# Kernel optimization log

Measured on AMD Instinct MI355X. Metric: run time of the kernel, lower is better.

## Reference

```python
import jax, jax.numpy as jnp
import numpy as np

D = 256          # embedding_dim
N_SUPPORT = 320  # n_way * n_shot = 20 * 16
N_QUERY = 2048
N_WAY = 20


def setup_inputs() -> dict:
    key = jax.random.key(0)
    ks = jax.random.split(key, 6)
    scale = 1.0 / np.sqrt(2 * D)
    return {
        "support_embeddings": jax.random.normal(ks[0], (N_SUPPORT, D), dtype=jnp.float32),
        "query_embeddings": jax.random.normal(ks[1], (N_QUERY, D), dtype=jnp.float32),
        "support_labels": jax.random.randint(ks[2], (N_SUPPORT,), 0, N_WAY, dtype=jnp.int64)
            if jax.config.jax_enable_x64 else jax.random.randint(ks[2], (N_SUPPORT,), 0, N_WAY, dtype=jnp.int32),
        "W1": jax.random.normal(ks[3], (2 * D, D), dtype=jnp.float32) * scale,
        "b1": jax.random.normal(ks[4], (D,), dtype=jnp.float32) * scale,
        "W2": jax.random.normal(ks[5], (D,), dtype=jnp.float32) * (1.0 / np.sqrt(D)),
        "b2": jnp.zeros((1,), dtype=jnp.float32),
        "n_way": N_WAY,
        "n_shot": 16,
    }


def reference(support_embeddings, query_embeddings, support_labels, W1, b1, W2, b2, n_way, n_shot):
    d = support_embeddings.shape[-1]
    # Linear1 over concat([query, support]) == query @ W1[:d] + support @ W1[d:]
    q_proj = query_embeddings @ W1[:d]          # [Q, D]
    s_proj = support_embeddings @ W1[d:]        # [S, D]
    hidden = jax.nn.relu(q_proj[:, None, :] + s_proj[None, :, :] + b1)  # [Q, S, D]
    scores = jnp.einsum("qsd,d->qs", hidden, W2) + b2[0]                # [Q, S]
    weights = jax.nn.softmax(scores, axis=1)                            # softmax over support set
    onehot = jax.nn.one_hot(support_labels, n_way, dtype=weights.dtype) # [S, n_way]
    logits = weights @ onehot                                           # [Q, n_way]
    return logits
```

## Files before the change

### kernel.cpp

```cpp
#include <hip/hip_runtime.h>
#include <cstdint>

#define DD   256
#define NS   320
#define NQ   2048
#define NWAY 20
#define QTP  8
#define NSP  2
#define SBLK 160
#define QT   4
#define CMAX 64

typedef _Float16 f16x2 __attribute__((ext_vector_type(2)));

__device__ __forceinline__ f16x2 u2f(unsigned u) {
  f16x2 f; __builtin_memcpy(&f, &u, 4); return f;
}

__device__ __forceinline__ float relu_dot2(f16x2 q, f16x2 s, f16x2 w, float c) {
  f16x2 h = q + s;
  const f16x2 z = {(_Float16)0.f, (_Float16)0.f};
  h = __builtin_elementwise_max(h, z);
#if __has_builtin(__builtin_amdgcn_fdot2)
  return __builtin_amdgcn_fdot2(h, w, c, false);
#else
  return c + (float)h.x * (float)w.x + (float)h.y * (float)w.y;
#endif
}

__global__ __launch_bounds__(1024) void proj_kernel(
    const float* __restrict__ sup, const float* __restrict__ qe,
    const float* __restrict__ W1, const float* __restrict__ b1,
    const float* __restrict__ W2,
    _Float16* __restrict__ qph, f16x2* __restrict__ spb2,
    _Float16* __restrict__ w2h) {
  __shared__ float pacc[3][QTP + NSP][DD];
  const int t  = threadIdx.x;
  const int d  = t & 255;
  const int kq = t >> 8;
  const int b  = blockIdx.x;
  const int r0 = b * QTP;
  const bool hasS = (b < SBLK);
  const int s0 = hasS ? b * NSP : 0;

  const float* wq = W1 + (size_t)(kq * 64) * DD + d;
  const float* ws = wq + (size_t)DD * DD;
  const float* qbase = qe  + __builtin_amdgcn_readfirstlane(r0 * DD + kq * 64);
  const float* sbase = sup + __builtin_amdgcn_readfirstlane(s0 * DD + kq * 64);

  if (b == 0 && kq == 0) w2h[d] = (_Float16)W2[d];

  float acc[QTP] = {};
  float accs[NSP] = {};
  if (hasS) {
#pragma unroll 8
    for (int k = 0; k < 64; ++k) {
      const float wv = wq[(size_t)k * DD];
#pragma unroll
      for (int i = 0; i < QTP; ++i)
        acc[i] += qbase[i * DD + k] * wv;
      const float wvs = ws[(size_t)k * DD];
      accs[0] += sbase[k] * wvs;
      accs[1] += sbase[DD + k] * wvs;
    }
  } else {
#pragma unroll 8
    for (int k = 0; k < 64; ++k) {
      const float wv = wq[(size_t)k * DD];
#pragma unroll
      for (int i = 0; i < QTP; ++i)
        acc[i] += qbase[i * DD + k] * wv;
    }
  }
  if (kq) {
#pragma unroll
    for (int i = 0; i < QTP; ++i) pacc[kq - 1][i][d] = acc[i];
    if (hasS) {
#pragma unroll
      for (int j = 0; j < NSP; ++j) pacc[kq - 1][QTP + j][d] = accs[j];
    }
  }
  __syncthreads();
  if (kq == 0) {
#pragma unroll
    for (int i = 0; i < QTP; ++i) {
      const float v = acc[i] + pacc[0][i][d] + pacc[1][i][d] + pacc[2][i][d];
      qph[(size_t)(r0 + i) * DD + d] = (_Float16)v;
    }
    if (hasS) {
      const float bb = b1[d];
#pragma unroll
      for (int j = 0; j < NSP; ++j) {
        const float v = accs[j] + pacc[0][QTP + j][d] + pacc[1][QTP + j][d] +
                        pacc[2][QTP + j][d] + bb;
        const float vh = __shfl_down(v, 1);
        if (!(d & 1)) {
          f16x2 p = {(_Float16)v, (_Float16)vh};
          spb2[(size_t)(d >> 1) * NS + (s0 + j)] = p;
        }
      }
    }
  }
}

__global__ __launch_bounds__(640) void matchnet_kernel(
    const _Float16* __restrict__ qph, const f16x2* __restrict__ spb2,
    const _Float16* __restrict__ w2h, const int* __restrict__ labels,
    float* __restrict__ out) {
  __shared__ float wexp[QT][NS];
  __shared__ float wm[5];
  __shared__ float csum[QT * NWAY];
  __shared__ int   ccnt[NWAY];
  __shared__ short cidx[NWAY * CMAX];
  const int t    = threadIdx.x;
  const int q0   = blockIdx.x * QT;
  const int half = t / NS;
  const int s    = t - half * NS;

  if (t < NWAY) ccnt[t] = 0;
  __syncthreads();
  if (!half) {
    const int lab  = labels[s];
    const int slot = atomicAdd(&ccnt[lab], 1);
    cidx[lab * CMAX + slot] = (short)s;
  }

  const int d0 = half * (DD / 2);
  const _Float16* qb = qph + __builtin_amdgcn_readfirstlane(q0 * DD + d0);
  const _Float16* wb = w2h + d0;
  const f16x2*    sb = spb2 + (size_t)(d0 >> 1) * NS + s;

  float acc[QT] = {};
#pragma unroll 2
  for (int dd = 0; dd < DD / 2; dd += 8) {
    const int dp = dd >> 1;
    const f16x2 sv0 = sb[(dp + 0) * NS];
    const f16x2 sv1 = sb[(dp + 1) * NS];
    const f16x2 sv2 = sb[(dp + 2) * NS];
    const f16x2 sv3 = sb[(dp + 3) * NS];
    const uint4 wv = *reinterpret_cast<const uint4*>(wb + dd);
    const f16x2 w0 = u2f(wv.x), w1 = u2f(wv.y), w2 = u2f(wv.z), w3 = u2f(wv.w);
#pragma unroll
    for (int i = 0; i < QT; ++i) {
      const uint4 qv = *reinterpret_cast<const uint4*>(qb + i * DD + dd);
      float a = acc[i];
      a = relu_dot2(u2f(qv.x), sv0, w0, a);
      a = relu_dot2(u2f(qv.y), sv1, w1, a);
      a = relu_dot2(u2f(qv.z), sv2, w2, a);
      a = relu_dot2(u2f(qv.w), sv3, w3, a);
      acc[i] = a;
    }
  }

  if (half) {
#pragma unroll
    for (int i = 0; i < QT; ++i) wexp[i][s] = acc[i];
  }
  __syncthreads();
  float m = -1e30f;
  if (!half) {
#pragma unroll
    for (int i = 0; i < QT; ++i) { acc[i] += wexp[i][s]; m = fmaxf(m, acc[i]); }
#pragma unroll
    for (int off = 32; off > 0; off >>= 1)
      m = fmaxf(m, __shfl_xor(m, off));
    if ((t & 63) == 0) wm[t >> 6] = m;
  }
  __syncthreads();
  if (!half) {
    const float M = fmaxf(fmaxf(fmaxf(wm[0], wm[1]), fmaxf(wm[2], wm[3])), wm[4]);
#pragma unroll
    for (int i = 0; i < QT; ++i) wexp[i][s] = __expf(acc[i] - M);
  }
  __syncthreads();
  if (t < QT * NWAY) {
    const int i = t / NWAY, c = t - i * NWAY;
    const int n = ccnt[c];
    float sum = 0.f;
    for (int j = 0; j < n; ++j) sum += wexp[i][cidx[c * CMAX + j]];
    csum[t] = sum;
  }
  __syncthreads();
  if (t < QT * NWAY) {
    const int i = t / NWAY, c = t - i * NWAY;
    float tot = 0.f;
#pragma unroll
    for (int j = 0; j < NWAY; ++j) tot += csum[i * NWAY + j];
    out[(size_t)(q0 + i) * NWAY + c] = csum[t] / tot;
  }
}

extern "C" void kernel_launch(void* const* d_in, const int* in_sizes, int n_in,
                              void* d_out, int out_size, void* d_ws, size_t ws_size,
                              hipStream_t stream) {
  const float* sup = (const float*)d_in[0];
  const float* qe  = (const float*)d_in[1];
  const int*   lab = (const int*)d_in[2];
  const float* W1  = (const float*)d_in[3];
  const float* b1  = (const float*)d_in[4];
  const float* W2  = (const float*)d_in[5];
  float* out = (float*)d_out;
  char* ws = (char*)d_ws;
  f16x2*    spb2 = (f16x2*)ws;
  _Float16* qph  = (_Float16*)(ws + 256 * 1024);
  _Float16* w2h  = (_Float16*)(ws + 256 * 1024 + 1024 * 1024);

  proj_kernel<<<NQ / QTP, 1024, 0, stream>>>(sup, qe, W1, b1, W2, qph, spb2, w2h);
  matchnet_kernel<<<NQ / QT, 640, 0, stream>>>(qph, spb2, w2h, lab, out);
}
```

Measured before the change: 91.10 us.

## Fuse projection and matching kernels with a grid-wide spin barrier

Merges the projection and matching kernels into one persistent launch of 256 blocks. Each block keeps its 8 query projections and W2 in LDS instead of writing them to global memory and reading them back. A global counter and flag barrier makes every block wait until all support projections are written before matching starts. The aim is to remove the second launch and the global round trip for the query projections. In exchange, all blocks must be co-resident, which the dynamic shared-memory pad is meant to control, and the flag and counter left over from a previous call could let blocks pass the barrier too early.

```diff
diff --git a/kernel.cpp b/kernel.cpp
--- a/kernel.cpp
+++ b/kernel.cpp
@@ -8,8 +8,9 @@
 #define QTP  8
 #define NSP  2
 #define SBLK 160
-#define QT   4
+#define NBLK 256
 #define CMAX 64
+#define MAGICF 0x1357BEEF0DDC0FFEULL
 
 typedef _Float16 f16x2 __attribute__((ext_vector_type(2)));
 
@@ -28,27 +29,44 @@
 #endif
 }
 
-__global__ __launch_bounds__(1024) void proj_kernel(
+__global__ __launch_bounds__(1024, 4) void fused_kernel(
     const float* __restrict__ sup, const float* __restrict__ qe,
     const float* __restrict__ W1, const float* __restrict__ b1,
-    const float* __restrict__ W2,
-    _Float16* __restrict__ qph, f16x2* __restrict__ spb2,
-    _Float16* __restrict__ w2h) {
+    const float* __restrict__ W2, const int* __restrict__ labels,
+    f16x2* __restrict__ spb2, unsigned long long* __restrict__ flag,
+    unsigned int* __restrict__ cnt, float* __restrict__ out) {
   __shared__ float pacc[3][QTP + NSP][DD];
-  const int t  = threadIdx.x;
+  __shared__ _Float16 qlds[QTP][DD];
+  __shared__ _Float16 w2l[DD];
+  __shared__ float wexp[QTP][NS];
+  __shared__ float wm[5];
+  __shared__ float csum[QTP * NWAY];
+  __shared__ int   ccnt[NWAY];
+  __shared__ short cidx[NWAY * CMAX];
+  extern __shared__ char occupancy_pad[];
+
+  const int t = threadIdx.x;
+  const int b = blockIdx.x;
+
+  if (b == 0 && t == 0) {
+    __hip_atomic_store(cnt, 0u, __ATOMIC_RELAXED, __HIP_MEMORY_SCOPE_AGENT);
+    __threadfence();
+    __hip_atomic_store(flag, (unsigned long long)MAGICF, __ATOMIC_RELEASE,
+                       __HIP_MEMORY_SCOPE_AGENT);
+  }
+
   const int d  = t & 255;
   const int kq = t >> 8;
-  const int b  = blockIdx.x;
   const int r0 = b * QTP;
   const bool hasS = (b < SBLK);
   const int s0 = hasS ? b * NSP : 0;
 
   const float* wq = W1 + (size_t)(kq * 64) * DD + d;
-  const float* ws = wq + (size_t)DD * DD;
+  const float* wsup = wq + (size_t)DD * DD;
   const float* qbase = qe  + __builtin_amdgcn_readfirstlane(r0 * DD + kq * 64);
   const float* sbase = sup + __builtin_amdgcn_readfirstlane(s0 * DD + kq * 64);
 
-  if (b == 0 && kq == 0) w2h[d] = (_Float16)W2[d];
+  if (kq == 0) w2l[d] = (_Float16)W2[d];
 
   float acc[QTP] = {};
   float accs[NSP] = {};
@@ -59,7 +77,7 @@
 #pragma unroll
       for (int i = 0; i < QTP; ++i)
         acc[i] += qbase[i * DD + k] * wv;
-      const float wvs = ws[(size_t)k * DD];
+      const float wvs = wsup[(size_t)k * DD];
       accs[0] += sbase[k] * wvs;
       accs[1] += sbase[DD + k] * wvs;
     }
@@ -85,7 +103,7 @@
 #pragma unroll
     for (int i = 0; i < QTP; ++i) {
       const float v = acc[i] + pacc[0][i][d] + pacc[1][i][d] + pacc[2][i][d];
-      qph[(size_t)(r0 + i) * DD + d] = (_Float16)v;
+      qlds[i][d] = (_Float16)v;
     }
     if (hasS) {
       const float bb = b1[d];
@@ -101,79 +119,80 @@
       }
     }
   }
-}
-
-__global__ __launch_bounds__(640) void matchnet_kernel(
-    const _Float16* __restrict__ qph, const f16x2* __restrict__ spb2,
-    const _Float16* __restrict__ w2h, const int* __restrict__ labels,
-    float* __restrict__ out) {
-  __shared__ float wexp[QT][NS];
-  __shared__ float wm[5];
-  __shared__ float csum[QT * NWAY];
-  __shared__ int   ccnt[NWAY];
-  __shared__ short cidx[NWAY * CMAX];
-  const int t    = threadIdx.x;
-  const int q0   = blockIdx.x * QT;
+
+  if (t < NWAY) ccnt[t] = 0;
+  __syncthreads();
+  if (t == 0) {
+    __threadfence();
+    int g = 0;
+    while (__hip_atomic_load(flag, __ATOMIC_ACQUIRE,
+                             __HIP_MEMORY_SCOPE_AGENT) != MAGICF &&
+           ++g < (1 << 24)) __builtin_amdgcn_s_sleep(2);
+    atomicAdd(cnt, 1u);
+    g = 0;
+    while (__hip_atomic_load(cnt, __ATOMIC_RELAXED,
+                             __HIP_MEMORY_SCOPE_AGENT) < NBLK &&
+           ++g < (1 << 24)) __builtin_amdgcn_s_sleep(2);
+    __threadfence();
+  }
+  __syncthreads();
+
   const int half = t / NS;
   const int s    = t - half * NS;
-
-  if (t < NWAY) ccnt[t] = 0;
-  __syncthreads();
-  if (!half) {
+  if (half == 0) {
     const int lab  = labels[s];
     const int slot = atomicAdd(&ccnt[lab], 1);
     cidx[lab * CMAX + slot] = (short)s;
   }
 
-  const int d0 = half * (DD / 2);
-  const _Float16* qb = qph + __builtin_amdgcn_readfirstlane(q0 * DD + d0);
-  const _Float16* wb = w2h + d0;
-  const f16x2*    sb = spb2 + (size_t)(d0 >> 1) * NS + s;
-
-  float acc[QT] = {};
+  float acc2[QTP] = {};
+  if (half < 2) {
+    const int d0 = half * (DD / 2);
+    const f16x2* sb = spb2 + (size_t)(d0 >> 1) * NS + s;
 #pragma unroll 2
-  for (int dd = 0; dd < DD / 2; dd += 8) {
-    const int dp = dd >> 1;
-    const f16x2 sv0 = sb[(dp + 0) * NS];
-    const f16x2 sv1 = sb[(dp + 1) * NS];
-    const f16x2 sv2 = sb[(dp + 2) * NS];
-    const f16x2 sv3 = sb[(dp + 3) * NS];
-    const uint4 wv = *reinterpret_cast<const uint4*>(wb + dd);
-    const f16x2 w0 = u2f(wv.x), w1 = u2f(wv.y), w2 = u2f(wv.z), w3 = u2f(wv.w);
-#pragma unroll
-    for (int i = 0; i < QT; ++i) {
-      const uint4 qv = *reinterpret_cast<const uint4*>(qb + i * DD + dd);
-      float a = acc[i];
-      a = relu_dot2(u2f(qv.x), sv0, w0, a);
-      a = relu_dot2(u2f(qv.y), sv1, w1, a);
-      a = relu_dot2(u2f(qv.z), sv2, w2, a);
-      a = relu_dot2(u2f(qv.w), sv3, w3, a);
-      acc[i] = a;
-    }
-  }
-
-  if (half) {
-#pragma unroll
-    for (int i = 0; i < QT; ++i) wexp[i][s] = acc[i];
+    for (int dd = 0; dd < DD / 2; dd += 8) {
+      const int dp = dd >> 1;
+      const f16x2 sv0 = sb[(dp + 0) * NS];
+      const f16x2 sv1 = sb[(dp + 1) * NS];
+      const f16x2 sv2 = sb[(dp + 2) * NS];
+      const f16x2 sv3 = sb[(dp + 3) * NS];
+      const uint4 wv = *reinterpret_cast<const uint4*>(&w2l[d0 + dd]);
+      const f16x2 w0 = u2f(wv.x), w1 = u2f(wv.y), w2v = u2f(wv.z), w3 = u2f(wv.w);
+#pragma unroll
+      for (int i = 0; i < QTP; ++i) {
+        const uint4 qv = *reinterpret_cast<const uint4*>(&qlds[i][d0 + dd]);
+        float a = acc2[i];
+        a = relu_dot2(u2f(qv.x), sv0, w0, a);
+        a = relu_dot2(u2f(qv.y), sv1, w1, a);
+        a = relu_dot2(u2f(qv.z), sv2, w2v, a);
+        a = relu_dot2(u2f(qv.w), sv3, w3, a);
+        acc2[i] = a;
+      }
+    }
+  }
+
+  if (half == 1) {
+#pragma unroll
+    for (int i = 0; i < QTP; ++i) wexp[i][s] = acc2[i];
   }
   __syncthreads();
   float m = -1e30f;
-  if (!half) {
-#pragma unroll
-    for (int i = 0; i < QT; ++i) { acc[i] += wexp[i][s]; m = fmaxf(m, acc[i]); }
+  if (half == 0) {
+#pragma unroll
+    for (int i = 0; i < QTP; ++i) { acc2[i] += wexp[i][s]; m = fmaxf(m, acc2[i]); }
 #pragma unroll
     for (int off = 32; off > 0; off >>= 1)
       m = fmaxf(m, __shfl_xor(m, off));
     if ((t & 63) == 0) wm[t >> 6] = m;
   }
   __syncthreads();
-  if (!half) {
+  if (half == 0) {
     const float M = fmaxf(fmaxf(fmaxf(wm[0], wm[1]), fmaxf(wm[2], wm[3])), wm[4]);
 #pragma unroll
-    for (int i = 0; i < QT; ++i) wexp[i][s] = __expf(acc[i] - M);
-  }
-  __syncthreads();
-  if (t < QT * NWAY) {
+    for (int i = 0; i < QTP; ++i) wexp[i][s] = __expf(acc2[i] - M);
+  }
+  __syncthreads();
+  if (t < QTP * NWAY) {
     const int i = t / NWAY, c = t - i * NWAY;
     const int n = ccnt[c];
     float sum = 0.f;
@@ -181,12 +200,12 @@
     csum[t] = sum;
   }
   __syncthreads();
-  if (t < QT * NWAY) {
+  if (t < QTP * NWAY) {
     const int i = t / NWAY, c = t - i * NWAY;
     float tot = 0.f;
 #pragma unroll
     for (int j = 0; j < NWAY; ++j) tot += csum[i * NWAY + j];
-    out[(size_t)(q0 + i) * NWAY + c] = csum[t] / tot;
+    out[(size_t)(b * QTP + i) * NWAY + c] = csum[t] / tot;
   }
 }
 
@@ -200,11 +219,11 @@
   const float* b1  = (const float*)d_in[4];
   const float* W2  = (const float*)d_in[5];
   float* out = (float*)d_out;
-  char* ws = (char*)d_ws;
-  f16x2*    spb2 = (f16x2*)ws;
-  _Float16* qph  = (_Float16*)(ws + 256 * 1024);
-  _Float16* w2h  = (_Float16*)(ws + 256 * 1024 + 1024 * 1024);
-
-  proj_kernel<<<NQ / QTP, 1024, 0, stream>>>(sup, qe, W1, b1, W2, qph, spb2, w2h);
-  matchnet_kernel<<<NQ / QT, 640, 0, stream>>>(qph, spb2, w2h, lab, out);
-}
+  char* wsp = (char*)d_ws;
+  f16x2* spb2 = (f16x2*)wsp;
+  unsigned long long* flag = (unsigned long long*)(wsp + 256 * 1024);
+  unsigned int* cnt = (unsigned int*)(wsp + 256 * 1024 + 8);
+
+  fused_kernel<<<NBLK, 1024, 41 * 1024, stream>>>(sup, qe, W1, b1, W2, lab,
+                                                  spb2, flag, cnt, out);
+}
```

Result: slower. 118.2 us (+29.8%).
